# Kernel tuning notes

Measured on AMD Instinct MI355X. Metric: run time of the kernel, lower is better.

## Reference

```python
import jax, jax.numpy as jnp
import numpy as np

B, T, D = 4, 4096, 1024
H = 16
DH = D // H
F = 4096
EPS = 1e-5


def _layernorm(x, gamma, beta):
    mu = jnp.mean(x, axis=-1, keepdims=True)
    var = jnp.var(x, axis=-1, keepdims=True)
    return (x - mu) * jax.lax.rsqrt(var + EPS) * gamma + beta


def setup_inputs() -> dict:
    key = jax.random.key(0)
    ks = jax.random.split(key, 10)
    s = 0.02
    return {
        "x": jax.random.normal(ks[0], (B, T, D), dtype=jnp.float32),
        "Wqkv": jax.random.normal(ks[1], (D, 3 * D), dtype=jnp.float32) * s,
        "bqkv": jnp.zeros((3 * D,), dtype=jnp.float32),
        "Wo": jax.random.normal(ks[2], (D, D), dtype=jnp.float32) * s,
        "bo": jnp.zeros((D,), dtype=jnp.float32),
        "W1": jax.random.normal(ks[3], (D, F), dtype=jnp.float32) * s,
        "b1": jnp.zeros((F,), dtype=jnp.float32),
        "W2": jax.random.normal(ks[4], (F, D), dtype=jnp.float32) * s,
        "b2": jnp.zeros((D,), dtype=jnp.float32),
        "g1": jnp.ones((D,), dtype=jnp.float32),
        "be1": jnp.zeros((D,), dtype=jnp.float32),
        "g2": jnp.ones((D,), dtype=jnp.float32),
        "be2": jnp.zeros((D,), dtype=jnp.float32),
    }


def reference(x, Wqkv, bqkv, Wo, bo, W1, b1, W2, b2, g1, be1, g2, be2):
    # fused QKV projection: [B,T,3D]
    qkv = jnp.einsum("btd,de->bte", x, Wqkv) + bqkv
    q, k, v = jnp.split(qkv, 3, axis=-1)
    # [B,H,T,DH]
    q = q.reshape(B, T, H, DH).transpose(0, 2, 1, 3)
    k = k.reshape(B, T, H, DH).transpose(0, 2, 1, 3)
    v = v.reshape(B, T, H, DH).transpose(0, 2, 1, 3)
    scores = jnp.einsum("bhqd,bhkd->bhqk", q, k) / jnp.sqrt(jnp.float32(DH))
    attn = jax.nn.softmax(scores, axis=-1)
    ctx = jnp.einsum("bhqk,bhkd->bhqd", attn, v)
    ctx = ctx.transpose(0, 2, 1, 3).reshape(B, T, D)
    # output projection + residual + post-LN
    x = _layernorm(x + (jnp.einsum("btd,de->bte", ctx, Wo) + bo), g1, be1)
    # FFN (exact GELU, torch default) + residual + post-LN
    h = jax.nn.gelu(jnp.einsum("btd,df->btf", x, W1) + b1, approximate=False)
    ffn = jnp.einsum("btf,fd->btd", h, W2) + b2
    return _layernorm(x + ffn, g2, be2)
```

## Files before the change

### kernel.cpp

```cpp
#include <hip/hip_runtime.h>
#include <math.h>

typedef unsigned short u16;
typedef unsigned int   u32;
typedef __attribute__((ext_vector_type(8))) short short8;
typedef __attribute__((ext_vector_type(4))) float f32x4;

#define B_  4
#define T_  4096
#define D_  1024
#define H_  16
#define DH_ 64
#define F_  4096
#define EPS_ 1e-5f
#define QKV_LD (3 * D_)

#define QSCALE_ 0.18033688011112042f

__device__ __forceinline__ float b2f(u16 v) {
    union { u32 u; float f; } x; x.u = ((u32)v) << 16; return x.f;
}
__device__ __forceinline__ u16 f2b(float f) {
    union { u32 u; float f; } x; x.f = f;
    u32 r = (x.u >> 16) & 1u;
    return (u16)((x.u + 0x7fffu + r) >> 16);
}
__device__ __forceinline__ u16 f2b_fast(float f) {
    union { u32 u; float f; } x; x.f = f;
    return (u16)((x.u + 0x8000u) >> 16);
}

__device__ __forceinline__ float ex2(float x) {
    float r;
    asm("v_exp_f32 %0, %1" : "=v"(r) : "v"(x));
    return r;
}
__device__ __forceinline__ float rcp_(float x) {
    float r;
    asm("v_rcp_f32 %0, %1" : "=v"(r) : "v"(x));
    return r;
}

__device__ __forceinline__ float gelu_erf(float x) {
    const float z = fabsf(x) * 0.70710678118654752f;
    const float t = rcp_(1.0f + 0.3275911f * z);
    float poly = 1.061405429f;
    poly = poly * t - 1.453152027f;
    poly = poly * t + 1.421413741f;
    poly = poly * t - 0.284496736f;
    poly = poly * t + 0.254829592f;
    poly = poly * t;
    const float e = ex2(-z * z * 1.4426950408889634f);
    const float erfz = 1.0f - poly * e;
    const float se = copysignf(erfz, x);
    return 0.5f * x * (1.0f + se);
}

__device__ __forceinline__ void gll16(const u16* g, u16* ldsbase) {
    __builtin_amdgcn_global_load_lds(
        (const __attribute__((address_space(1))) void*)g,
        (__attribute__((address_space(3))) void*)ldsbase, 16, 0, 0);
}

__global__ __launch_bounds__(256) void conv_bf16_kernel(
    const float* __restrict__ in, u16* __restrict__ out)
{
    const int i = blockIdx.x * 256 + threadIdx.x;
    float4 v = ((const float4*)in)[i];
    ushort4 o;
    o.x = f2b(v.x); o.y = f2b(v.y); o.z = f2b(v.z); o.w = f2b(v.w);
    ((ushort4*)out)[i] = o;
}

__global__ __launch_bounds__(256) void transpose_bf16_kernel(
    const float* __restrict__ W, u16* __restrict__ Wt, int R, int C)
{
    __shared__ float tile[32][33];
    const int bx = blockIdx.x * 32;
    const int by = blockIdx.y * 32;
    const int tx = threadIdx.x & 31, ty = threadIdx.x >> 5;
#pragma unroll
    for (int p = 0; p < 4; ++p)
        tile[ty + p * 8][tx] = W[(size_t)(by + ty + p * 8) * C + bx + tx];
    __syncthreads();
#pragma unroll
    for (int p = 0; p < 4; ++p)
        Wt[(size_t)(bx + ty + p * 8) * R + by + tx] = f2b(tile[tx][ty + p * 8]);
}

template<bool CBF>
__global__ __launch_bounds__(256) void mfma_gemm(
    const u16* __restrict__ A, int lda,
    const u16* __restrict__ Bt, int ldbt,
    const float* __restrict__ bias,
    void* __restrict__ Cv, int ldc,
    int K, int act, int acc, int qcols)
{
    __shared__ __align__(16) u16 Al[128 * 32];
    __shared__ __align__(16) u16 Bl[128 * 32];

    const int tid  = threadIdx.x;
    const int lane = tid & 63, wave = tid >> 6;
    const int quad = lane >> 4, l16 = lane & 15;
    const int m0 = blockIdx.y * 128, n0 = blockIdx.x * 128;
    const int wm = (wave >> 1) * 64, wn = (wave & 1) * 64;

    int srow[2], sgk[2];
#pragma unroll
    for (int t = 0; t < 2; ++t) {
        const int c = wave * 128 + t * 64 + lane;
        srow[t] = c >> 2;
        sgk[t] = ((c & 3) ^ ((srow[t] >> 1) & 3)) * 8;
    }
    const u16* Ag = A  + (size_t)m0 * lda;
    const u16* Bg = Bt + (size_t)n0 * ldbt;
    const int apos = (quad ^ ((l16 >> 1) & 3)) * 8;

    f32x4 accr[4][4];
#pragma unroll
    for (int i = 0; i < 4; ++i)
#pragma unroll
        for (int j = 0; j < 4; ++j)
            accr[i][j] = (f32x4)(0.0f);

    for (int k0 = 0; k0 < K; k0 += 32) {
        __syncthreads();
#pragma unroll
        for (int t = 0; t < 2; ++t) {
            gll16(Ag + (size_t)srow[t] * lda  + k0 + sgk[t], &Al[(wave * 128 + t * 64) * 8]);
            gll16(Bg + (size_t)srow[t] * ldbt + k0 + sgk[t], &Bl[(wave * 128 + t * 64) * 8]);
        }
        __syncthreads();

        short8 af[4], bf[4];
#pragma unroll
        for (int i = 0; i < 4; ++i)
            af[i] = *(const short8*)&Al[(wm + i * 16 + l16) * 32 + apos];
#pragma unroll
        for (int j = 0; j < 4; ++j)
            bf[j] = *(const short8*)&Bl[(wn + j * 16 + l16) * 32 + apos];
#pragma unroll
        for (int i = 0; i < 4; ++i)
#pragma unroll
            for (int j = 0; j < 4; ++j)
                accr[i][j] = __builtin_amdgcn_mfma_f32_16x16x32_bf16(
                    af[i], bf[j], accr[i][j], 0, 0, 0);
    }

#pragma unroll
    for (int j = 0; j < 4; ++j) {
        const int cc = n0 + wn + j * 16 + l16;
        float bv = acc ? 0.0f : bias[cc];
        const float sc = (cc < qcols) ? QSCALE_ : 1.0f;
#pragma unroll
        for (int i = 0; i < 4; ++i) {
#pragma unroll
            for (int r = 0; r < 4; ++r) {
                const int rr = m0 + wm + i * 16 + quad * 4 + r;
                float v = (accr[i][j][r] + bv) * sc;
                if (act == 1)
                    v = gelu_erf(v);
                if (CBF) {
                    ((u16*)Cv)[(size_t)rr * ldc + cc] = f2b(v);
                } else {
                    float* dst = (float*)Cv + (size_t)rr * ldc + cc;
                    if (acc) v += *dst;
                    *dst = v;
                }
            }
        }
    }
}

__global__ __launch_bounds__(256) void attn_mfma_kernel(
    const u16* __restrict__ qkv, u16* __restrict__ ctx)
{
    __shared__ u16 Ks[64 * 72];
    __shared__ u16 Vt[64 * 72];
    __shared__ u16 Ps[4][32 * 72];

    const int tid  = threadIdx.x;
    const int lane = tid & 63, wave = tid >> 6;
    const int quad = lane >> 4, l16 = lane & 15;
    const int b = blockIdx.z, h = blockIdx.y;
    const int q0 = blockIdx.x * 128;

    short8 ones8;
#pragma unroll
    for (int i = 0; i < 8; ++i) ones8[i] = (short)0x3F80;

    short8 aq[2][2];
    {
        const u16* qb = qkv + (size_t)(b * T_ + q0 + wave * 32) * QKV_LD + h * DH_;
#pragma unroll
        for (int u = 0; u < 2; ++u)
#pragma unroll
            for (int s = 0; s < 2; ++s)
                aq[u][s] = *(const short8*)(qb + (size_t)(u * 16 + l16) * QKV_LD + s * 32 + quad * 8);
    }

    const int srow = tid >> 3;
    const int scol = (tid & 7) * 8;
    const u16* kg = qkv + (size_t)(b * T_) * QKV_LD + D_     + h * DH_;
    const u16* vg = qkv + (size_t)(b * T_) * QKV_LD + 2 * D_ + h * DH_;

    short8 kreg[2], vreg[2];
#pragma unroll
    for (int half = 0; half < 2; ++half) {
        const int row = srow + half * 32;
        kreg[half] = *(const short8*)(kg + (size_t)row * QKV_LD + scol);
        vreg[half] = *(const short8*)(vg + (size_t)row * QKV_LD + scol);
    }

    f32x4 o_acc[2][4];
#pragma unroll
    for (int u = 0; u < 2; ++u)
#pragma unroll
        for (int nt = 0; nt < 4; ++nt)
            o_acc[u][nt] = (f32x4)(0.0f);
    f32x4 l_acc[2];
    l_acc[0] = (f32x4)(0.0f);
    l_acc[1] = (f32x4)(0.0f);

    for (int kt = 0; kt < T_; kt += 64) {
        __syncthreads();
#pragma unroll
        for (int half = 0; half < 2; ++half) {
            const int row = srow + half * 32;
            *(short8*)&Ks[row * 72 + scol] = kreg[half];
            u16* vd = &Vt[row ^ scol];
#pragma unroll
            for (int jj = 0; jj < 8; ++jj)
                vd[(scol + jj) * 72] = ((const u16*)&vreg[half])[jj];
        }
        __syncthreads();

        if (kt + 64 < T_) {
#pragma unroll
            for (int half = 0; half < 2; ++half) {
                const int row = srow + half * 32;
                kreg[half] = *(const short8*)(kg + (size_t)(kt + 64 + row) * QKV_LD + scol);
                vreg[half] = *(const short8*)(vg + (size_t)(kt + 64 + row) * QKV_LD + scol);
            }
        }

        f32x4 sa[2][4];
#pragma unroll
        for (int u = 0; u < 2; ++u)
#pragma unroll
            for (int nt = 0; nt < 4; ++nt)
                sa[u][nt] = (f32x4)(0.0f);
        __builtin_amdgcn_s_setprio(1);
#pragma unroll
        for (int s = 0; s < 2; ++s) {
            short8 kb[4];
#pragma unroll
            for (int nt = 0; nt < 4; ++nt)
                kb[nt] = *(const short8*)&Ks[(nt * 16 + l16) * 72 + s * 32 + quad * 8];
#pragma unroll
            for (int u = 0; u < 2; ++u)
#pragma unroll
                for (int nt = 0; nt < 4; ++nt)
                    sa[u][nt] = __builtin_amdgcn_mfma_f32_16x16x32_bf16(
                        aq[u][s], kb[nt], sa[u][nt], 0, 0, 0);
        }
        __builtin_amdgcn_s_setprio(0);

#pragma unroll
        for (int u = 0; u < 2; ++u) {
#pragma unroll
            for (int nt = 0; nt < 4; ++nt) {
#pragma unroll
                for (int r = 0; r < 4; ++r) {
                    float p = ex2(sa[u][nt][r]);
                    Ps[wave][(u * 16 + quad * 4 + r) * 72 + nt * 16 + l16] = f2b_fast(p);
                }
            }
        }

        __builtin_amdgcn_s_setprio(1);
#pragma unroll
        for (int s = 0; s < 2; ++s) {
            short8 pa[2];
#pragma unroll
            for (int u = 0; u < 2; ++u)
                pa[u] = *(const short8*)&Ps[wave][(u * 16 + l16) * 72 + s * 32 + quad * 8];
#pragma unroll
            for (int u = 0; u < 2; ++u)
                l_acc[u] = __builtin_amdgcn_mfma_f32_16x16x32_bf16(
                    pa[u], ones8, l_acc[u], 0, 0, 0);
#pragma unroll
            for (int nt = 0; nt < 4; ++nt) {
                const int dh = nt * 16 + l16;
                short8 vb = *(const short8*)&Vt[dh * 72 + ((s * 32 + quad * 8) ^ (dh & 56))];
#pragma unroll
                for (int u = 0; u < 2; ++u)
                    o_acc[u][nt] = __builtin_amdgcn_mfma_f32_16x16x32_bf16(
                        pa[u], vb, o_acc[u][nt], 0, 0, 0);
            }
        }
        __builtin_amdgcn_s_setprio(0);
    }

#pragma unroll
    for (int u = 0; u < 2; ++u) {
#pragma unroll
        for (int r = 0; r < 4; ++r) {
            const float inv = 1.0f / l_acc[u][r];
            const size_t row = (size_t)(b * T_ + q0 + wave * 32 + u * 16 + quad * 4 + r);
#pragma unroll
            for (int nt = 0; nt < 4; ++nt)
                ctx[row * D_ + h * DH_ + nt * 16 + l16] = f2b(o_acc[u][nt][r] * inv);
        }
    }
}

template<bool ABF, bool BBF, bool OBF>
__global__ __launch_bounds__(256) void add_ln_kernel(
    const void* __restrict__ av, const void* __restrict__ bv,
    const float* __restrict__ g, const float* __restrict__ be,
    void* __restrict__ outv)
{
    const int row = blockIdx.x;
    const int tid = threadIdx.x;

    float v[4];
    if (ABF) {
        ushort4 va = *(const ushort4*)((const u16*)av + (size_t)row * D_ + tid * 4);
        v[0] = b2f(va.x); v[1] = b2f(va.y); v[2] = b2f(va.z); v[3] = b2f(va.w);
    } else {
        float4 va = *(const float4*)((const float*)av + (size_t)row * D_ + tid * 4);
        v[0] = va.x; v[1] = va.y; v[2] = va.z; v[3] = va.w;
    }
    if (BBF) {
        ushort4 vb = *(const ushort4*)((const u16*)bv + (size_t)row * D_ + tid * 4);
        v[0] += b2f(vb.x); v[1] += b2f(vb.y); v[2] += b2f(vb.z); v[3] += b2f(vb.w);
    } else {
        float4 vb = *(const float4*)((const float*)bv + (size_t)row * D_ + tid * 4);
        v[0] += vb.x; v[1] += vb.y; v[2] += vb.z; v[3] += vb.w;
    }

    float s  = v[0] + v[1] + v[2] + v[3];
    float ss = v[0]*v[0] + v[1]*v[1] + v[2]*v[2] + v[3]*v[3];
#pragma unroll
    for (int off = 32; off > 0; off >>= 1) {
        s  += __shfl_down(s,  off, 64);
        ss += __shfl_down(ss, off, 64);
    }
    __shared__ float ws[4], wss[4], stats[2];
    const int wave = tid >> 6, lane = tid & 63;
    if (lane == 0) { ws[wave] = s; wss[wave] = ss; }
    __syncthreads();
    if (tid == 0) {
        float ts  = ws[0] + ws[1] + ws[2] + ws[3];
        float tss = wss[0] + wss[1] + wss[2] + wss[3];
        float mu  = ts * (1.0f / D_);
        float var = tss * (1.0f / D_) - mu * mu;
        stats[0] = mu;
        stats[1] = rsqrtf(var + EPS_);
    }
    __syncthreads();
    const float mu = stats[0], rs = stats[1];

    const float4 g4  = *(const float4*)(g  + tid * 4);
    const float4 be4 = *(const float4*)(be + tid * 4);
    float gg[4]  = {g4.x, g4.y, g4.z, g4.w};
    float beb[4] = {be4.x, be4.y, be4.z, be4.w};
    if (OBF) {
        ushort4 o;
        o.x = f2b((v[0] - mu) * rs * gg[0] + beb[0]);
        o.y = f2b((v[1] - mu) * rs * gg[1] + beb[1]);
        o.z = f2b((v[2] - mu) * rs * gg[2] + beb[2]);
        o.w = f2b((v[3] - mu) * rs * gg[3] + beb[3]);
        *(ushort4*)((u16*)outv + (size_t)row * D_ + tid * 4) = o;
    } else {
        float4 o;
        o.x = (v[0] - mu) * rs * gg[0] + beb[0];
        o.y = (v[1] - mu) * rs * gg[1] + beb[1];
        o.z = (v[2] - mu) * rs * gg[2] + beb[2];
        o.w = (v[3] - mu) * rs * gg[3] + beb[3];
        *(float4*)((float*)outv + (size_t)row * D_ + tid * 4) = o;
    }
}

extern "C" void kernel_launch(void* const* d_in, const int* in_sizes, int n_in,
                              void* d_out, int out_size, void* d_ws, size_t ws_size,
                              hipStream_t stream)
{
    const float* x    = (const float*)d_in[0];
    const float* Wqkv = (const float*)d_in[1];
    const float* bqkv = (const float*)d_in[2];
    const float* Wo   = (const float*)d_in[3];
    const float* bo   = (const float*)d_in[4];
    const float* W1   = (const float*)d_in[5];
    const float* b1   = (const float*)d_in[6];
    const float* W2   = (const float*)d_in[7];
    const float* b2   = (const float*)d_in[8];
    const float* g1   = (const float*)d_in[9];
    const float* be1  = (const float*)d_in[10];
    const float* g2   = (const float*)d_in[11];
    const float* be2  = (const float*)d_in[12];
    float* out = (float*)d_out;

    const int M = B_ * T_;
    char* ws = (char*)d_ws;
    char* sc = (char*)d_out;

    u16*   qkvB   = (u16*)ws;
    u16*   ctxB   = (u16*)(ws + (size_t)100663296);
    float* proj   = (float*)ws;
    u16*   x1B    = (u16*)(ws + (size_t)100663296);
    u16*   hchunk = (u16*)ws;
    u16*   ffnB   = (u16*)(ws + (size_t)67108864);

    u16* xB    = (u16*)sc;
    u16* WqkvT = (u16*)(sc + (size_t)33554432);
    u16* WoT   = (u16*)(sc + (size_t)39845888);
    u16* W1T   = (u16*)(sc + (size_t)41943040);
    u16* W2T   = (u16*)(sc + (size_t)50331648);

    dim3 blk(256);

    conv_bf16_kernel<<<dim3(M * D_ / 1024), blk, 0, stream>>>(x, xB);
    transpose_bf16_kernel<<<dim3(3 * D_ / 32, D_ / 32), blk, 0, stream>>>(Wqkv, WqkvT, D_, 3 * D_);
    transpose_bf16_kernel<<<dim3(D_ / 32, D_ / 32), blk, 0, stream>>>(Wo, WoT, D_, D_);
    transpose_bf16_kernel<<<dim3(F_ / 32, D_ / 32), blk, 0, stream>>>(W1, W1T, D_, F_);
    transpose_bf16_kernel<<<dim3(D_ / 32, F_ / 32), blk, 0, stream>>>(W2, W2T, F_, D_);

    mfma_gemm<true><<<dim3(3 * D_ / 128, M / 128), blk, 0, stream>>>(
        xB, D_, WqkvT, D_, bqkv, qkvB, 3 * D_, D_, 0, 0, D_);

    attn_mfma_kernel<<<dim3(T_ / 128, H_, B_), blk, 0, stream>>>(qkvB, ctxB);

    mfma_gemm<false><<<dim3(D_ / 128, M / 128), blk, 0, stream>>>(
        ctxB, D_, WoT, D_, bo, proj, D_, D_, 0, 0, 0);

    add_ln_kernel<false, false, true><<<dim3(M), blk, 0, stream>>>(x, proj, g1, be1, x1B);

    for (int mc = 0; mc < 2; ++mc) {
        const size_t m0 = (size_t)mc * 8192;
        mfma_gemm<true><<<dim3(F_ / 128, 8192 / 128), blk, 0, stream>>>(
            x1B + m0 * D_, D_, W1T, D_, b1, hchunk, F_, D_, 1, 0, 0);
        mfma_gemm<true><<<dim3(D_ / 128, 8192 / 128), blk, 0, stream>>>(
            hchunk, F_, W2T, F_, b2, ffnB + m0 * D_, D_, F_, 0, 0, 0);
    }

    add_ln_kernel<true, true, false><<<dim3(M), blk, 0, stream>>>(x1B, ffnB, g2, be2, out);
}
```

Measured before the change: 1.159 ms.

## Remap workgroups across XCDs and double the K-step for the W2 GEMM

```diff
diff --git a/kernel.cpp b/kernel.cpp
--- a/kernel.cpp
+++ b/kernel.cpp
@@ -88,7 +88,7 @@
         Wt[(size_t)(bx + ty + p * 8) * R + by + tx] = f2b(tile[tx][ty + p * 8]);
 }
 
-template<bool CBF>
+template<bool CBF, int KU>
 __global__ __launch_bounds__(256) void mfma_gemm(
     const u16* __restrict__ A, int lda,
     const u16* __restrict__ Bt, int ldbt,
@@ -96,13 +96,19 @@
     void* __restrict__ Cv, int ldc,
     int K, int act, int acc, int qcols)
 {
-    __shared__ __align__(16) u16 Al[128 * 32];
-    __shared__ __align__(16) u16 Bl[128 * 32];
+    __shared__ __align__(16) u16 Al[KU][128 * 32];
+    __shared__ __align__(16) u16 Bl[KU][128 * 32];
 
     const int tid  = threadIdx.x;
     const int lane = tid & 63, wave = tid >> 6;
     const int quad = lane >> 4, l16 = lane & 15;
-    const int m0 = blockIdx.y * 128, n0 = blockIdx.x * 128;
+
+    const int gx = gridDim.x;
+    const int nwg = gx * gridDim.y;
+    const int lin = blockIdx.y * gx + blockIdx.x;
+    const int wg  = (lin & 7) * (nwg >> 3) + (lin >> 3);
+    const int m0 = (wg / gx) * 128, n0 = (wg % gx) * 128;
+
     const int wm = (wave >> 1) * 64, wn = (wave & 1) * 64;
 
     int srow[2], sgk[2];
@@ -123,28 +129,35 @@
         for (int j = 0; j < 4; ++j)
             accr[i][j] = (f32x4)(0.0f);
 
-    for (int k0 = 0; k0 < K; k0 += 32) {
+    for (int k0 = 0; k0 < K; k0 += 32 * KU) {
         __syncthreads();
 #pragma unroll
-        for (int t = 0; t < 2; ++t) {
-            gll16(Ag + (size_t)srow[t] * lda  + k0 + sgk[t], &Al[(wave * 128 + t * 64) * 8]);
-            gll16(Bg + (size_t)srow[t] * ldbt + k0 + sgk[t], &Bl[(wave * 128 + t * 64) * 8]);
-        }
+        for (int h = 0; h < KU; ++h)
+#pragma unroll
+            for (int t = 0; t < 2; ++t) {
+                gll16(Ag + (size_t)srow[t] * lda  + k0 + h * 32 + sgk[t],
+                      &Al[h][(wave * 128 + t * 64) * 8]);
+                gll16(Bg + (size_t)srow[t] * ldbt + k0 + h * 32 + sgk[t],
+                      &Bl[h][(wave * 128 + t * 64) * 8]);
+            }
         __syncthreads();
 
-        short8 af[4], bf[4];
-#pragma unroll
-        for (int i = 0; i < 4; ++i)
-            af[i] = *(const short8*)&Al[(wm + i * 16 + l16) * 32 + apos];
-#pragma unroll
-        for (int j = 0; j < 4; ++j)
-            bf[j] = *(const short8*)&Bl[(wn + j * 16 + l16) * 32 + apos];
-#pragma unroll
-        for (int i = 0; i < 4; ++i)
+#pragma unroll
+        for (int h = 0; h < KU; ++h) {
+            short8 af[4], bf[4];
+#pragma unroll
+            for (int i = 0; i < 4; ++i)
+                af[i] = *(const short8*)&Al[h][(wm + i * 16 + l16) * 32 + apos];
 #pragma unroll
             for (int j = 0; j < 4; ++j)
-                accr[i][j] = __builtin_amdgcn_mfma_f32_16x16x32_bf16(
-                    af[i], bf[j], accr[i][j], 0, 0, 0);
+                bf[j] = *(const short8*)&Bl[h][(wn + j * 16 + l16) * 32 + apos];
+#pragma unroll
+            for (int i = 0; i < 4; ++i)
+#pragma unroll
+                for (int j = 0; j < 4; ++j)
+                    accr[i][j] = __builtin_amdgcn_mfma_f32_16x16x32_bf16(
+                        af[i], bf[j], accr[i][j], 0, 0, 0);
+        }
     }
 
 #pragma unroll
@@ -182,8 +195,14 @@
     const int tid  = threadIdx.x;
     const int lane = tid & 63, wave = tid >> 6;
     const int quad = lane >> 4, l16 = lane & 15;
-    const int b = blockIdx.z, h = blockIdx.y;
-    const int q0 = blockIdx.x * 128;
+
+    const int gx = gridDim.x, gy = gridDim.y;
+    const int nwg = gx * gy * gridDim.z;
+    const int lin = (blockIdx.z * gy + blockIdx.y) * gx + blockIdx.x;
+    const int wg  = (lin & 7) * (nwg >> 3) + (lin >> 3);
+    const int q0 = (wg % gx) * 128;
+    const int h  = (wg / gx) % gy;
+    const int b  = wg / (gx * gy);
 
     short8 ones8;
 #pragma unroll
@@ -427,21 +446,21 @@
     transpose_bf16_kernel<<<dim3(F_ / 32, D_ / 32), blk, 0, stream>>>(W1, W1T, D_, F_);
     transpose_bf16_kernel<<<dim3(D_ / 32, F_ / 32), blk, 0, stream>>>(W2, W2T, F_, D_);
 
-    mfma_gemm<true><<<dim3(3 * D_ / 128, M / 128), blk, 0, stream>>>(
+    mfma_gemm<true, 1><<<dim3(3 * D_ / 128, M / 128), blk, 0, stream>>>(
         xB, D_, WqkvT, D_, bqkv, qkvB, 3 * D_, D_, 0, 0, D_);
 
     attn_mfma_kernel<<<dim3(T_ / 128, H_, B_), blk, 0, stream>>>(qkvB, ctxB);
 
-    mfma_gemm<false><<<dim3(D_ / 128, M / 128), blk, 0, stream>>>(
+    mfma_gemm<false, 1><<<dim3(D_ / 128, M / 128), blk, 0, stream>>>(
         ctxB, D_, WoT, D_, bo, proj, D_, D_, 0, 0, 0);
 
     add_ln_kernel<false, false, true><<<dim3(M), blk, 0, stream>>>(x, proj, g1, be1, x1B);
 
     for (int mc = 0; mc < 2; ++mc) {
         const size_t m0 = (size_t)mc * 8192;
-        mfma_gemm<true><<<dim3(F_ / 128, 8192 / 128), blk, 0, stream>>>(
+        mfma_gemm<true, 1><<<dim3(F_ / 128, 8192 / 128), blk, 0, stream>>>(
             x1B + m0 * D_, D_, W1T, D_, b1, hchunk, F_, D_, 1, 0, 0);
-        mfma_gemm<true><<<dim3(D_ / 128, 8192 / 128), blk, 0, stream>>>(
+        mfma_gemm<true, 2><<<dim3(D_ / 128, 8192 / 128), blk, 0, stream>>>(
             hchunk, F_, W2T, F_, b2, ffnB + m0 * D_, D_, F_, 0, 0, 0);
     }
 
```

After: 1.092 ms. 1.06x faster.
